# Kernel optimization log

Measured on AMD Instinct MI355X. Metric: run time of the kernel, lower is better.

Reference implementation:

```python
import jax, jax.numpy as jnp
import numpy as np

N = 50000       # node_num
E = 800000      # edges (no self loops; reference adds them)
IN_C = 128
OUT_C = 128
HEADS = 1
NEG_SLOPE = 0.2
BN_EPS = 1e-5


def setup_inputs() -> dict:
    key = jax.random.key(0)
    ks = jax.random.split(key, 12)
    x = jax.random.normal(ks[0], (N, IN_C), dtype=jnp.float32)
    # edge_index with no self-loops: dst = (src + off) % N, off in [1, N)
    src = jax.random.randint(ks[1], (E,), 0, N)
    off = jax.random.randint(ks[2], (E,), 1, N)
    dst = (src + off) % N
    edge_index = jnp.stack([src, dst]).astype(jnp.int64)
    embedding = jax.random.normal(ks[3], (N, OUT_C), dtype=jnp.float32)
    s = 1.0 / np.sqrt(IN_C)
    lin_w = jax.random.uniform(ks[4], (HEADS * OUT_C, IN_C), jnp.float32, -s, s)
    g = 0.1
    att_i = jax.random.normal(ks[5], (1, HEADS, OUT_C), jnp.float32) * g
    att_j = jax.random.normal(ks[6], (1, HEADS, OUT_C), jnp.float32) * g
    att_em_i = jax.random.normal(ks[7], (1, HEADS, OUT_C), jnp.float32) * g
    att_em_j = jax.random.normal(ks[8], (1, HEADS, OUT_C), jnp.float32) * g
    bias = jnp.zeros((OUT_C,), jnp.float32)
    gamma = jnp.ones((OUT_C,), jnp.float32)
    beta = jnp.zeros((OUT_C,), jnp.float32)
    return {"x": x, "edge_index": edge_index, "embedding": embedding,
            "lin_w": lin_w, "att_i": att_i, "att_j": att_j,
            "att_em_i": att_em_i, "att_em_j": att_em_j,
            "bias": bias, "gamma": gamma, "beta": beta}


def _gnn_forward(x, embedding, lin_w, att_i, att_j, att_em_i, att_em_j,
                 bias, gamma, beta, src, dst):
    n = x.shape[0]
    xl = (x @ lin_w.T).reshape(n, HEADS, OUT_C)          # [N,H,C]
    x_j = xl[src]                                         # [E',H,C] source
    x_i = xl[dst]                                         # [E',H,C] target
    emb_i = embedding[dst][:, None, :]                    # [E',1,C]
    emb_j = embedding[src][:, None, :]
    # alpha_e = <[x_i||emb_i], [att_i||att_em_i]> + <[x_j||emb_j], [att_j||att_em_j]>
    alpha = ((x_i * att_i).sum(-1) + (emb_i * att_em_i).sum(-1)
             + (x_j * att_j).sum(-1) + (emb_j * att_em_j).sum(-1))  # [E',H]
    alpha = jnp.where(alpha >= 0, alpha, NEG_SLOPE * alpha)         # leaky_relu
    # segment softmax over destination node (PyG softmax)
    amax = jax.ops.segment_max(alpha, dst, num_segments=n)
    ex = jnp.exp(alpha - amax[dst])
    denom = jax.ops.segment_sum(ex, dst, num_segments=n)
    alpha = ex / (denom[dst] + 1e-16)                               # [E',H]
    out = jax.ops.segment_sum(x_j * alpha[..., None], dst, num_segments=n)  # [N,H,C]
    out = out.mean(axis=1) + bias                                   # concat=False
    # BatchNorm1d, training mode (biased batch variance)
    mu = out.mean(axis=0)
    var = ((out - mu) ** 2).mean(axis=0)
    return (out - mu) * jax.lax.rsqrt(var + BN_EPS) * gamma + beta


def reference(x, edge_index, embedding, lin_w, att_i, att_j,
              att_em_i, att_em_j, bias, gamma, beta):
    n = x.shape[0]
    loops = jnp.arange(n, dtype=edge_index.dtype)
    src = jnp.concatenate([edge_index[0], loops])
    dst = jnp.concatenate([edge_index[1], loops])
    return _gnn_forward(x, embedding, lin_w, att_i, att_j, att_em_i,
                        att_em_j, bias, gamma, beta, src, dst)
```

## Files before the change

kernel.cpp:

```cpp
#include <hip/hip_runtime.h>

typedef short bf16x8 __attribute__((ext_vector_type(8)));
typedef float f32x4 __attribute__((ext_vector_type(4)));

__device__ __forceinline__ unsigned short f2bf(float f) {
  unsigned int u = __float_as_uint(f);
  u += 0x7fffu + ((u >> 16) & 1u);
  return (unsigned short)(u >> 16);
}
__device__ __forceinline__ float bf2f(unsigned short h) {
  return __uint_as_float(((unsigned int)h) << 16);
}
__device__ __forceinline__ float lrelu(float a) { return a >= 0.f ? a : 0.2f * a; }

#define BN_PS 1568

__global__ void zero_kernel(int* __restrict__ p, int n) {
  int i = blockIdx.x * blockDim.x + threadIdx.x;
  int stride = gridDim.x * blockDim.x;
  for (; i < n; i += stride) p[i] = 0;
}

__global__ __launch_bounds__(256) void gemm_kernel(
    const float* __restrict__ x, const float* __restrict__ w,
    const float* __restrict__ emb,
    const float* __restrict__ att_i, const float* __restrict__ att_j,
    const float* __restrict__ att_em_i, const float* __restrict__ att_em_j,
    unsigned short* __restrict__ xl, float* __restrict__ ai, float* __restrict__ aj,
    int n) {
  __shared__ __align__(16) unsigned short xs[64 * 128];
  __shared__ __align__(16) unsigned short wl[128 * 128];
  const int t = threadIdx.x;
  const int r0 = blockIdx.x * 64;
#pragma unroll
  for (int i = 0; i < 16; ++i) {
    int f4 = t + i * 256;
    int row = f4 >> 5;
    int kk = (f4 & 31) << 2;
    float4 v = *(const float4*)(w + row * 128 + kk);
    ushort4 b;
    b.x = f2bf(v.x); b.y = f2bf(v.y); b.z = f2bf(v.z); b.w = f2bf(v.w);
    int boff = (kk << 1) ^ ((row & 7) << 4);
    *(ushort4*)((char*)wl + row * 256 + boff) = b;
  }
#pragma unroll
  for (int i = 0; i < 8; ++i) {
    int f4 = t + i * 256;
    int row = f4 >> 5;
    int kk = (f4 & 31) << 2;
    int gr = r0 + row;
    float4 v;
    if (gr < n) v = *(const float4*)(x + gr * 128 + kk);
    else { v.x = 0.f; v.y = 0.f; v.z = 0.f; v.w = 0.f; }
    ushort4 b;
    b.x = f2bf(v.x); b.y = f2bf(v.y); b.z = f2bf(v.z); b.w = f2bf(v.w);
    int boff = (kk << 1) ^ ((row & 7) << 4);
    *(ushort4*)((char*)xs + row * 256 + boff) = b;
  }
  __syncthreads();
  const int wid = t >> 6, lane = t & 63;
  const int m16 = lane & 15, kg = lane >> 4;
  const int arow = wid * 16 + m16;
  const f32x4 vzero = {0.f, 0.f, 0.f, 0.f};
  f32x4 acc[8];
#pragma unroll
  for (int i = 0; i < 8; ++i) acc[i] = vzero;
#pragma unroll
  for (int s = 0; s < 4; ++s) {
    int kb = s * 64 + kg * 16;
    bf16x8 a = *(const bf16x8*)((const char*)xs + arow * 256 + (kb ^ ((arow & 7) << 4)));
#pragma unroll
    for (int cf = 0; cf < 8; ++cf) {
      int wrow = cf * 16 + m16;
      bf16x8 b = *(const bf16x8*)((const char*)wl + wrow * 256 + (kb ^ ((wrow & 7) << 4)));
      acc[cf] = __builtin_amdgcn_mfma_f32_16x16x32_bf16(a, b, acc[cf], 0, 0, 0);
    }
  }
  const int crow0 = wid * 16 + kg * 4;
#pragma unroll
  for (int q = 0; q < 4; ++q) {
    int gr = r0 + crow0 + q;
    if (gr < n) {
#pragma unroll
      for (int cf = 0; cf < 8; ++cf)
        xl[gr * 128 + cf * 16 + m16] = f2bf(acc[cf][q]);
    }
  }
  float ati[8], atj[8];
#pragma unroll
  for (int cf = 0; cf < 8; ++cf) {
    ati[cf] = att_i[cf * 16 + m16];
    atj[cf] = att_j[cf * 16 + m16];
  }
  float4 aemi0 = *(const float4*)(att_em_i + m16 * 8);
  float4 aemi1 = *(const float4*)(att_em_i + m16 * 8 + 4);
  float4 aemj0 = *(const float4*)(att_em_j + m16 * 8);
  float4 aemj1 = *(const float4*)(att_em_j + m16 * 8 + 4);
#pragma unroll
  for (int q = 0; q < 4; ++q) {
    int gr = r0 + crow0 + q;
    if (gr < n) {
      float si = 0.f, sj = 0.f;
#pragma unroll
      for (int cf = 0; cf < 8; ++cf) {
        si += acc[cf][q] * ati[cf];
        sj += acc[cf][q] * atj[cf];
      }
      const float* ep = emb + (size_t)gr * 128 + m16 * 8;
      float4 e0 = *(const float4*)(ep);
      float4 e1 = *(const float4*)(ep + 4);
      si += e0.x * aemi0.x + e0.y * aemi0.y + e0.z * aemi0.z + e0.w * aemi0.w
          + e1.x * aemi1.x + e1.y * aemi1.y + e1.z * aemi1.z + e1.w * aemi1.w;
      sj += e0.x * aemj0.x + e0.y * aemj0.y + e0.z * aemj0.z + e0.w * aemj0.w
          + e1.x * aemj1.x + e1.y * aemj1.y + e1.z * aemj1.z + e1.w * aemj1.w;
#pragma unroll
      for (int off = 1; off < 16; off <<= 1) {
        si += __shfl_xor(si, off);
        sj += __shfl_xor(sj, off);
      }
      if (m16 == 0) { ai[gr] = si; aj[gr] = sj; }
    }
  }
}

__global__ __launch_bounds__(256) void count_rank_kernel(
    const int* __restrict__ dst, int* __restrict__ cnt, int* __restrict__ pw, int E) {
  int e = (blockIdx.x * blockDim.x + threadIdx.x) * 4;
  if (e + 3 < E) {
    int4 d4 = *(const int4*)(dst + e);
    int4 p4;
    p4.x = atomicAdd(&cnt[d4.x], 1);
    p4.y = atomicAdd(&cnt[d4.y], 1);
    p4.z = atomicAdd(&cnt[d4.z], 1);
    p4.w = atomicAdd(&cnt[d4.w], 1);
    *(int4*)(pw + e) = p4;
  } else {
    for (; e < E; ++e) pw[e] = atomicAdd(&cnt[dst[e]], 1);
  }
}

__global__ __launch_bounds__(1024) void scan1_kernel(
    const int* __restrict__ cnt, int* __restrict__ rp, int* __restrict__ bsum, int n) {
  __shared__ int wsum[16];
  int t = threadIdx.x, lane = t & 63, wid = t >> 6;
  int i = blockIdx.x * 1024 + t;
  int v = (i < n) ? cnt[i] : 0;
  int incl = v;
#pragma unroll
  for (int off = 1; off < 64; off <<= 1) {
    int u = __shfl_up(incl, off);
    if (lane >= off) incl += u;
  }
  if (lane == 63) wsum[wid] = incl;
  __syncthreads();
  if (t < 16) {
    int wv = wsum[t];
    int winc = wv;
#pragma unroll
    for (int off = 1; off < 16; off <<= 1) {
      int u = __shfl_up(winc, off);
      if (t >= off) winc += u;
    }
    wsum[t] = winc - wv;
  }
  __syncthreads();
  int excl = wsum[wid] + incl - v;
  if (i < n) rp[i] = excl;
  if (t == 1023) bsum[blockIdx.x] = excl + v;
}

__global__ __launch_bounds__(64) void scan2_kernel(
    int* __restrict__ bsum, int* __restrict__ rp, int nb, int n) {
  int t = threadIdx.x;
  int carry = 0;
  for (int base = 0; base < nb; base += 64) {
    int idx = base + t;
    int v = (idx < nb) ? bsum[idx] : 0;
    int incl = v;
#pragma unroll
    for (int off = 1; off < 64; off <<= 1) {
      int u = __shfl_up(incl, off);
      if (t >= off) incl += u;
    }
    if (idx < nb) bsum[idx] = carry + incl - v;
    carry += __shfl(incl, 63);
  }
  if (t == 0) rp[n] = carry;
}

__global__ __launch_bounds__(256) void scan3_kernel(
    const int* __restrict__ bsum, int* __restrict__ rp, int n) {
  int i = blockIdx.x * blockDim.x + threadIdx.x;
  if (i < n) rp[i] += bsum[i >> 10];
}

__global__ __launch_bounds__(256) void scatter_kernel(
    const int* __restrict__ src, const int* __restrict__ dst,
    const int* __restrict__ rp, const int* __restrict__ pw,
    int* __restrict__ csr, int E) {
  int e = (blockIdx.x * blockDim.x + threadIdx.x) * 4;
  if (e + 3 < E) {
    int4 s4 = *(const int4*)(src + e);
    int4 d4 = *(const int4*)(dst + e);
    int4 p4 = *(const int4*)(pw + e);
    int r0 = rp[d4.x], r1 = rp[d4.y], r2 = rp[d4.z], r3 = rp[d4.w];
    csr[r0 + p4.x] = s4.x;
    csr[r1 + p4.y] = s4.y;
    csr[r2 + p4.z] = s4.z;
    csr[r3 + p4.w] = s4.w;
  } else {
    for (; e < E; ++e) csr[rp[dst[e]] + pw[e]] = src[e];
  }
}

__global__ __launch_bounds__(256) void agg_kernel(
    const float* __restrict__ ai, const float* __restrict__ aj,
    const unsigned short* __restrict__ xl,
    const int* __restrict__ row_ptr, const int* __restrict__ csr_src,
    const float* __restrict__ bias, float* __restrict__ out, int n) {
  int wid = threadIdx.x >> 6, lane = threadIdx.x & 63;
  int node = blockIdx.x * 4 + wid;
  if (node >= n) return;
  int beg = row_ptr[node], end = row_ptr[node + 1];
  float ain = ai[node];
  float w_self = __expf(lrelu(ain + aj[node]));
  float dl = 0.f;
  float acc0 = 0.f, acc1 = 0.f;
  const int c0 = lane * 2;
  for (int cs = beg; cs < end; cs += 64) {
    int ce = min(64, end - cs);
    int s = 0;
    float we = 0.f;
    if (lane < ce) {
      s = csr_src[cs + lane];
      we = __expf(lrelu(ain + aj[s]));
    }
    dl += we;
    int j = 0;
    for (; j + 8 <= ce; j += 8) {
      float w0 = __shfl(we, j),     w1 = __shfl(we, j + 1);
      float w2 = __shfl(we, j + 2), w3 = __shfl(we, j + 3);
      float w4 = __shfl(we, j + 4), w5 = __shfl(we, j + 5);
      float w6 = __shfl(we, j + 6), w7 = __shfl(we, j + 7);
      int i0 = __shfl(s, j),     i1 = __shfl(s, j + 1);
      int i2 = __shfl(s, j + 2), i3 = __shfl(s, j + 3);
      int i4 = __shfl(s, j + 4), i5 = __shfl(s, j + 5);
      int i6 = __shfl(s, j + 6), i7 = __shfl(s, j + 7);
      ushort2 v0 = *(const ushort2*)(xl + (size_t)i0 * 128 + c0);
      ushort2 v1 = *(const ushort2*)(xl + (size_t)i1 * 128 + c0);
      ushort2 v2 = *(const ushort2*)(xl + (size_t)i2 * 128 + c0);
      ushort2 v3 = *(const ushort2*)(xl + (size_t)i3 * 128 + c0);
      ushort2 v4 = *(const ushort2*)(xl + (size_t)i4 * 128 + c0);
      ushort2 v5 = *(const ushort2*)(xl + (size_t)i5 * 128 + c0);
      ushort2 v6 = *(const ushort2*)(xl + (size_t)i6 * 128 + c0);
      ushort2 v7 = *(const ushort2*)(xl + (size_t)i7 * 128 + c0);
      acc0 += w0 * bf2f(v0.x); acc1 += w0 * bf2f(v0.y);
      acc0 += w1 * bf2f(v1.x); acc1 += w1 * bf2f(v1.y);
      acc0 += w2 * bf2f(v2.x); acc1 += w2 * bf2f(v2.y);
      acc0 += w3 * bf2f(v3.x); acc1 += w3 * bf2f(v3.y);
      acc0 += w4 * bf2f(v4.x); acc1 += w4 * bf2f(v4.y);
      acc0 += w5 * bf2f(v5.x); acc1 += w5 * bf2f(v5.y);
      acc0 += w6 * bf2f(v6.x); acc1 += w6 * bf2f(v6.y);
      acc0 += w7 * bf2f(v7.x); acc1 += w7 * bf2f(v7.y);
    }
    for (; j < ce; ++j) {
      float wj = __shfl(we, j);
      int ij = __shfl(s, j);
      ushort2 v = *(const ushort2*)(xl + (size_t)ij * 128 + c0);
      acc0 += wj * bf2f(v.x); acc1 += wj * bf2f(v.y);
    }
  }
#pragma unroll
  for (int off = 32; off > 0; off >>= 1) dl += __shfl_xor(dl, off);
  float inv = 1.f / (dl + w_self + 1e-16f);
  ushort2 u = *(const ushort2*)(xl + (size_t)node * 128 + c0);
  float2 o;
  o.x = (acc0 + w_self * bf2f(u.x)) * inv + bias[c0];
  o.y = (acc1 + w_self * bf2f(u.y)) * inv + bias[c0 + 1];
  *(float2*)(out + (size_t)node * 128 + c0) = o;
}

__global__ __launch_bounds__(256) void bnstat_a_kernel(
    const float* __restrict__ out, float* __restrict__ pS, float* __restrict__ pQ,
    int n) {
  __shared__ float4 red_s[8][32];
  __shared__ float4 red_q[8][32];
  int q = threadIdx.x & 31;
  int rs = threadIdx.x >> 5;
  int rbase = blockIdx.x * 32;
  float4 s = {0.f, 0.f, 0.f, 0.f}, ss = {0.f, 0.f, 0.f, 0.f};
#pragma unroll
  for (int k = 0; k < 4; ++k) {
    int r = rbase + rs + k * 8;
    if (r < n) {
      float4 v = *(const float4*)(out + (size_t)r * 128 + q * 4);
      s.x += v.x; s.y += v.y; s.z += v.z; s.w += v.w;
      ss.x += v.x * v.x; ss.y += v.y * v.y; ss.z += v.z * v.z; ss.w += v.w * v.w;
    }
  }
  red_s[rs][q] = s;
  red_q[rs][q] = ss;
  __syncthreads();
  if (threadIdx.x < 32) {
    float4 ts = red_s[0][threadIdx.x], tq = red_q[0][threadIdx.x];
#pragma unroll
    for (int k = 1; k < 8; ++k) {
      float4 a = red_s[k][threadIdx.x], b = red_q[k][threadIdx.x];
      ts.x += a.x; ts.y += a.y; ts.z += a.z; ts.w += a.w;
      tq.x += b.x; tq.y += b.y; tq.z += b.z; tq.w += b.w;
    }
    int c = threadIdx.x * 4;
    int b = blockIdx.x;
    pS[(c + 0) * BN_PS + b] = ts.x; pS[(c + 1) * BN_PS + b] = ts.y;
    pS[(c + 2) * BN_PS + b] = ts.z; pS[(c + 3) * BN_PS + b] = ts.w;
    pQ[(c + 0) * BN_PS + b] = tq.x; pQ[(c + 1) * BN_PS + b] = tq.y;
    pQ[(c + 2) * BN_PS + b] = tq.z; pQ[(c + 3) * BN_PS + b] = tq.w;
  }
}

__global__ __launch_bounds__(256) void bnstat_b_kernel(
    const float* __restrict__ pS, const float* __restrict__ pQ,
    float* __restrict__ sums, float* __restrict__ sumsq, int nb) {
  __shared__ float ws_s[4], ws_q[4];
  int c = blockIdx.x;
  int t = threadIdx.x, lane = t & 63, wid = t >> 6;
  const float* rowS = pS + (size_t)c * BN_PS;
  const float* rowQ = pQ + (size_t)c * BN_PS;
  float s = 0.f, qv = 0.f;
  for (int i = t; i < nb; i += 256) {
    s += rowS[i];
    qv += rowQ[i];
  }
#pragma unroll
  for (int off = 32; off > 0; off >>= 1) {
    s += __shfl_xor(s, off);
    qv += __shfl_xor(qv, off);
  }
  if (lane == 0) { ws_s[wid] = s; ws_q[wid] = qv; }
  __syncthreads();
  if (t == 0) {
    sums[c] = ws_s[0] + ws_s[1] + ws_s[2] + ws_s[3];
    sumsq[c] = ws_q[0] + ws_q[1] + ws_q[2] + ws_q[3];
  }
}

__global__ __launch_bounds__(256) void bnapply_kernel(
    float* __restrict__ out, const float* __restrict__ sums,
    const float* __restrict__ sumsq, const float* __restrict__ gamma,
    const float* __restrict__ beta, int n, float invN) {
  int q = threadIdx.x & 31;
  int rs = threadIdx.x >> 5;
  int c = q * 4;
  float4 mu, var, sc, sh;
  mu.x = sums[c + 0] * invN; mu.y = sums[c + 1] * invN;
  mu.z = sums[c + 2] * invN; mu.w = sums[c + 3] * invN;
  var.x = sumsq[c + 0] * invN - mu.x * mu.x;
  var.y = sumsq[c + 1] * invN - mu.y * mu.y;
  var.z = sumsq[c + 2] * invN - mu.z * mu.z;
  var.w = sumsq[c + 3] * invN - mu.w * mu.w;
  sc.x = rsqrtf(var.x + 1e-5f) * gamma[c + 0];
  sc.y = rsqrtf(var.y + 1e-5f) * gamma[c + 1];
  sc.z = rsqrtf(var.z + 1e-5f) * gamma[c + 2];
  sc.w = rsqrtf(var.w + 1e-5f) * gamma[c + 3];
  sh.x = beta[c + 0] - mu.x * sc.x;
  sh.y = beta[c + 1] - mu.y * sc.y;
  sh.z = beta[c + 2] - mu.z * sc.z;
  sh.w = beta[c + 3] - mu.w * sc.w;
  for (int r = blockIdx.x * 8 + rs; r < n; r += gridDim.x * 8) {
    float4 v = *(const float4*)(out + (size_t)r * 128 + c);
    v.x = v.x * sc.x + sh.x;
    v.y = v.y * sc.y + sh.y;
    v.z = v.z * sc.z + sh.z;
    v.w = v.w * sc.w + sh.w;
    *(float4*)(out + (size_t)r * 128 + c) = v;
  }
}

extern "C" void kernel_launch(void* const* d_in, const int* in_sizes, int n_in,
                              void* d_out, int out_size, void* d_ws, size_t ws_size,
                              hipStream_t stream) {
  (void)n_in; (void)out_size; (void)ws_size;
  const float* x = (const float*)d_in[0];
  const int* ei = (const int*)d_in[1];
  const float* emb = (const float*)d_in[2];
  const float* lin_w = (const float*)d_in[3];
  const float* att_i = (const float*)d_in[4];
  const float* att_j = (const float*)d_in[5];
  const float* att_em_i = (const float*)d_in[6];
  const float* att_em_j = (const float*)d_in[7];
  const float* bias = (const float*)d_in[8];
  const float* gamma = (const float*)d_in[9];
  const float* beta = (const float*)d_in[10];
  float* out = (float*)d_out;
  const int N = in_sizes[0] / 128;
  const int E = in_sizes[1] / 2;
  const int* src = ei;
  const int* dst = ei + E;
  const int NB = (N + 1023) / 1024;
  const int NBA = (N + 31) / 32;

  auto align_up = [](size_t v) { return (v + 255) & ~(size_t)255; };
  size_t off = 0;
  size_t xl_off = off;    off = align_up(off + (size_t)N * 128 * 2);
  size_t ai_off = off;    off = align_up(off + (size_t)N * 4);
  size_t aj_off = off;    off = align_up(off + (size_t)N * 4);
  size_t rp_off = off;    off = align_up(off + (size_t)(N + 1) * 4);
  size_t csr_off = off;   off = align_up(off + (size_t)E * 4);
  size_t pw_off = off;    off = align_up(off + (size_t)E * 4);
  size_t bsum_off = off;  off = align_up(off + (size_t)(NB + 1) * 4);
  size_t pS_off = off;    off = align_up(off + (size_t)128 * BN_PS * 4);
  size_t pQ_off = off;    off = align_up(off + (size_t)128 * BN_PS * 4);
  size_t sums_off = off;  off = align_up(off + 512);
  size_t sumsq_off = off; off = align_up(off + 512);
  size_t cnt_off = off;   off = align_up(off + (size_t)N * 4);

  char* ws = (char*)d_ws;
  unsigned short* xl = (unsigned short*)(ws + xl_off);
  float* ai = (float*)(ws + ai_off);
  float* aj = (float*)(ws + aj_off);
  int* rp = (int*)(ws + rp_off);
  int* csr = (int*)(ws + csr_off);
  int* pw = (int*)(ws + pw_off);
  int* bsum = (int*)(ws + bsum_off);
  float* pS = (float*)(ws + pS_off);
  float* pQ = (float*)(ws + pQ_off);
  float* sums = (float*)(ws + sums_off);
  float* sumsq = (float*)(ws + sumsq_off);
  int* cnt = (int*)(ws + cnt_off);

  hipLaunchKernelGGL(zero_kernel, dim3((N + 255) / 256), dim3(256), 0, stream,
                     cnt, N);
  hipLaunchKernelGGL(gemm_kernel, dim3((N + 63) / 64), dim3(256), 0, stream,
                     x, lin_w, emb, att_i, att_j, att_em_i, att_em_j,
                     xl, ai, aj, N);
  hipLaunchKernelGGL(count_rank_kernel, dim3((E / 4 + 255) / 256), dim3(256), 0, stream,
                     dst, cnt, pw, E);
  hipLaunchKernelGGL(scan1_kernel, dim3(NB), dim3(1024), 0, stream, cnt, rp, bsum, N);
  hipLaunchKernelGGL(scan2_kernel, dim3(1), dim3(64), 0, stream, bsum, rp, NB, N);
  hipLaunchKernelGGL(scan3_kernel, dim3((N + 255) / 256), dim3(256), 0, stream,
                     bsum, rp, N);
  hipLaunchKernelGGL(scatter_kernel, dim3((E / 4 + 255) / 256), dim3(256), 0, stream,
                     src, dst, rp, pw, csr, E);
  hipLaunchKernelGGL(agg_kernel, dim3((N + 3) / 4), dim3(256), 0, stream,
                     ai, aj, xl, rp, csr, bias, out, N);
  hipLaunchKernelGGL(bnstat_a_kernel, dim3(NBA), dim3(256), 0, stream,
                     out, pS, pQ, N);
  hipLaunchKernelGGL(bnstat_b_kernel, dim3(128), dim3(256), 0, stream,
                     pS, pQ, sums, sumsq, NBA);
  hipLaunchKernelGGL(bnapply_kernel, dim3(2048), dim3(256), 0, stream,
                     out, sums, sumsq, gamma, beta, N, 1.0f / (float)N);
}
```

Before: 240.2 us.

## Fuse edge counting into GEMM launch, merge scans, fold BN stats into aggregation

Edge-count atomics now run as extra blocks of the GEMM kernel, so both overlap in one launch. The two-stage block-prefix scan is merged into a single kernel where each block recomputes its prefix with wave reductions. BatchNorm partial sums are computed inside the aggregation kernel, which removes a full reread of the output. It also prefetches the next CSR chunk and widens scatter to 8 edges per thread. The cost is redundant per-block prefix work and a larger partial-sum buffer (one entry per 4 nodes) for bnstat_b to reduce.

```diff
diff --git a/kernel.cpp b/kernel.cpp
--- a/kernel.cpp
+++ b/kernel.cpp
@@ -13,23 +13,44 @@
 }
 __device__ __forceinline__ float lrelu(float a) { return a >= 0.f ? a : 0.2f * a; }
 
-#define BN_PS 1568
-
 __global__ void zero_kernel(int* __restrict__ p, int n) {
   int i = blockIdx.x * blockDim.x + threadIdx.x;
   int stride = gridDim.x * blockDim.x;
   for (; i < n; i += stride) p[i] = 0;
 }
 
-__global__ __launch_bounds__(256) void gemm_kernel(
+__global__ __launch_bounds__(256) void gemm_cnt_kernel(
     const float* __restrict__ x, const float* __restrict__ w,
     const float* __restrict__ emb,
     const float* __restrict__ att_i, const float* __restrict__ att_j,
     const float* __restrict__ att_em_i, const float* __restrict__ att_em_j,
     unsigned short* __restrict__ xl, float* __restrict__ ai, float* __restrict__ aj,
-    int n) {
+    int n,
+    const int* __restrict__ dst, int* __restrict__ cnt, int* __restrict__ pw, int E,
+    int NBG) {
   __shared__ __align__(16) unsigned short xs[64 * 128];
   __shared__ __align__(16) unsigned short wl[128 * 128];
+  if (blockIdx.x >= NBG) {
+    int e = ((blockIdx.x - NBG) * blockDim.x + threadIdx.x) * 8;
+    if (e + 8 <= E) {
+      int4 d0 = *(const int4*)(dst + e);
+      int4 d1 = *(const int4*)(dst + e + 4);
+      int4 p0, p1;
+      p0.x = atomicAdd(&cnt[d0.x], 1);
+      p0.y = atomicAdd(&cnt[d0.y], 1);
+      p0.z = atomicAdd(&cnt[d0.z], 1);
+      p0.w = atomicAdd(&cnt[d0.w], 1);
+      p1.x = atomicAdd(&cnt[d1.x], 1);
+      p1.y = atomicAdd(&cnt[d1.y], 1);
+      p1.z = atomicAdd(&cnt[d1.z], 1);
+      p1.w = atomicAdd(&cnt[d1.w], 1);
+      *(int4*)(pw + e) = p0;
+      *(int4*)(pw + e + 4) = p1;
+    } else {
+      for (; e < E; ++e) pw[e] = atomicAdd(&cnt[dst[e]], 1);
+    }
+    return;
+  }
   const int t = threadIdx.x;
   const int r0 = blockIdx.x * 64;
 #pragma unroll
@@ -123,22 +144,6 @@
   }
 }
 
-__global__ __launch_bounds__(256) void count_rank_kernel(
-    const int* __restrict__ dst, int* __restrict__ cnt, int* __restrict__ pw, int E) {
-  int e = (blockIdx.x * blockDim.x + threadIdx.x) * 4;
-  if (e + 3 < E) {
-    int4 d4 = *(const int4*)(dst + e);
-    int4 p4;
-    p4.x = atomicAdd(&cnt[d4.x], 1);
-    p4.y = atomicAdd(&cnt[d4.y], 1);
-    p4.z = atomicAdd(&cnt[d4.z], 1);
-    p4.w = atomicAdd(&cnt[d4.w], 1);
-    *(int4*)(pw + e) = p4;
-  } else {
-    for (; e < E; ++e) pw[e] = atomicAdd(&cnt[dst[e]], 1);
-  }
-}
-
 __global__ __launch_bounds__(1024) void scan1_kernel(
     const int* __restrict__ cnt, int* __restrict__ rp, int* __restrict__ bsum, int n) {
   __shared__ int wsum[16];
@@ -169,45 +174,50 @@
   if (t == 1023) bsum[blockIdx.x] = excl + v;
 }
 
-__global__ __launch_bounds__(64) void scan2_kernel(
-    int* __restrict__ bsum, int* __restrict__ rp, int nb, int n) {
-  int t = threadIdx.x;
-  int carry = 0;
+__global__ __launch_bounds__(256) void scan3_kernel(
+    const int* __restrict__ bsum, int* __restrict__ rp, int n, int nb) {
+  int lane = threadIdx.x & 63;
+  int bb = blockIdx.x >> 2;
+  int pref = 0, tot = 0;
   for (int base = 0; base < nb; base += 64) {
-    int idx = base + t;
+    int idx = base + lane;
     int v = (idx < nb) ? bsum[idx] : 0;
-    int incl = v;
-#pragma unroll
-    for (int off = 1; off < 64; off <<= 1) {
-      int u = __shfl_up(incl, off);
-      if (t >= off) incl += u;
-    }
-    if (idx < nb) bsum[idx] = carry + incl - v;
-    carry += __shfl(incl, 63);
-  }
-  if (t == 0) rp[n] = carry;
-}
-
-__global__ __launch_bounds__(256) void scan3_kernel(
-    const int* __restrict__ bsum, int* __restrict__ rp, int n) {
-  int i = blockIdx.x * blockDim.x + threadIdx.x;
-  if (i < n) rp[i] += bsum[i >> 10];
+    int p = (idx < bb) ? v : 0;
+#pragma unroll
+    for (int off = 32; off > 0; off >>= 1) {
+      p += __shfl_xor(p, off);
+      v += __shfl_xor(v, off);
+    }
+    pref += p;
+    tot += v;
+  }
+  int i = blockIdx.x * 256 + threadIdx.x;
+  if (i < n) rp[i] += pref;
+  if (blockIdx.x == gridDim.x - 1 && threadIdx.x == 0) rp[n] = tot;
 }
 
 __global__ __launch_bounds__(256) void scatter_kernel(
     const int* __restrict__ src, const int* __restrict__ dst,
     const int* __restrict__ rp, const int* __restrict__ pw,
     int* __restrict__ csr, int E) {
-  int e = (blockIdx.x * blockDim.x + threadIdx.x) * 4;
-  if (e + 3 < E) {
-    int4 s4 = *(const int4*)(src + e);
-    int4 d4 = *(const int4*)(dst + e);
-    int4 p4 = *(const int4*)(pw + e);
-    int r0 = rp[d4.x], r1 = rp[d4.y], r2 = rp[d4.z], r3 = rp[d4.w];
-    csr[r0 + p4.x] = s4.x;
-    csr[r1 + p4.y] = s4.y;
-    csr[r2 + p4.z] = s4.z;
-    csr[r3 + p4.w] = s4.w;
+  int e = (blockIdx.x * blockDim.x + threadIdx.x) * 8;
+  if (e + 8 <= E) {
+    int4 s0 = *(const int4*)(src + e);
+    int4 s1 = *(const int4*)(src + e + 4);
+    int4 d0 = *(const int4*)(dst + e);
+    int4 d1 = *(const int4*)(dst + e + 4);
+    int4 p0 = *(const int4*)(pw + e);
+    int4 p1 = *(const int4*)(pw + e + 4);
+    int r0 = rp[d0.x], r1 = rp[d0.y], r2 = rp[d0.z], r3 = rp[d0.w];
+    int r4 = rp[d1.x], r5 = rp[d1.y], r6 = rp[d1.z], r7 = rp[d1.w];
+    csr[r0 + p0.x] = s0.x;
+    csr[r1 + p0.y] = s0.y;
+    csr[r2 + p0.z] = s0.z;
+    csr[r3 + p0.w] = s0.w;
+    csr[r4 + p1.x] = s1.x;
+    csr[r5 + p1.y] = s1.y;
+    csr[r6 + p1.z] = s1.z;
+    csr[r7 + p1.w] = s1.w;
   } else {
     for (; e < E; ++e) csr[rp[dst[e]] + pw[e]] = src[e];
   }
@@ -217,25 +227,32 @@
     const float* __restrict__ ai, const float* __restrict__ aj,
     const unsigned short* __restrict__ xl,
     const int* __restrict__ row_ptr, const int* __restrict__ csr_src,
-    const float* __restrict__ bias, float* __restrict__ out, int n) {
+    const float* __restrict__ bias, float* __restrict__ out,
+    float* __restrict__ pS, float* __restrict__ pQ, int n, int ps2) {
+  __shared__ float2 red_s[4][64];
+  __shared__ float2 red_q[4][64];
   int wid = threadIdx.x >> 6, lane = threadIdx.x & 63;
   int node = blockIdx.x * 4 + wid;
-  if (node >= n) return;
-  int beg = row_ptr[node], end = row_ptr[node + 1];
-  float ain = ai[node];
-  float w_self = __expf(lrelu(ain + aj[node]));
-  float dl = 0.f;
-  float acc0 = 0.f, acc1 = 0.f;
+  bool active = node < n;
+  int beg = 0, end = 0;
+  float ain = 0.f, w_self = 0.f;
+  if (active) {
+    beg = row_ptr[node];
+    end = row_ptr[node + 1];
+    ain = ai[node];
+    w_self = __expf(lrelu(ain + aj[node]));
+  }
+  float dl = 0.f, acc0 = 0.f, acc1 = 0.f;
   const int c0 = lane * 2;
+  int s = 0;
+  if (beg + lane < end) s = csr_src[beg + lane];
   for (int cs = beg; cs < end; cs += 64) {
     int ce = min(64, end - cs);
-    int s = 0;
     float we = 0.f;
-    if (lane < ce) {
-      s = csr_src[cs + lane];
-      we = __expf(lrelu(ain + aj[s]));
-    }
+    if (lane < ce) we = __expf(lrelu(ain + aj[s]));
     dl += we;
+    int s_nxt = 0;
+    if (cs + 64 + lane < end) s_nxt = csr_src[cs + 64 + lane];
     int j = 0;
     for (; j + 8 <= ce; j += 8) {
       float w0 = __shfl(we, j),     w1 = __shfl(we, j + 1);
@@ -269,63 +286,47 @@
       ushort2 v = *(const ushort2*)(xl + (size_t)ij * 128 + c0);
       acc0 += wj * bf2f(v.x); acc1 += wj * bf2f(v.y);
     }
+    s = s_nxt;
   }
 #pragma unroll
   for (int off = 32; off > 0; off >>= 1) dl += __shfl_xor(dl, off);
   float inv = 1.f / (dl + w_self + 1e-16f);
-  ushort2 u = *(const ushort2*)(xl + (size_t)node * 128 + c0);
-  float2 o;
-  o.x = (acc0 + w_self * bf2f(u.x)) * inv + bias[c0];
-  o.y = (acc1 + w_self * bf2f(u.y)) * inv + bias[c0 + 1];
-  *(float2*)(out + (size_t)node * 128 + c0) = o;
-}
-
-__global__ __launch_bounds__(256) void bnstat_a_kernel(
-    const float* __restrict__ out, float* __restrict__ pS, float* __restrict__ pQ,
-    int n) {
-  __shared__ float4 red_s[8][32];
-  __shared__ float4 red_q[8][32];
-  int q = threadIdx.x & 31;
-  int rs = threadIdx.x >> 5;
-  int rbase = blockIdx.x * 32;
-  float4 s = {0.f, 0.f, 0.f, 0.f}, ss = {0.f, 0.f, 0.f, 0.f};
-#pragma unroll
-  for (int k = 0; k < 4; ++k) {
-    int r = rbase + rs + k * 8;
-    if (r < n) {
-      float4 v = *(const float4*)(out + (size_t)r * 128 + q * 4);
-      s.x += v.x; s.y += v.y; s.z += v.z; s.w += v.w;
-      ss.x += v.x * v.x; ss.y += v.y * v.y; ss.z += v.z * v.z; ss.w += v.w * v.w;
-    }
-  }
-  red_s[rs][q] = s;
-  red_q[rs][q] = ss;
+  float2 o; o.x = 0.f; o.y = 0.f;
+  if (active) {
+    ushort2 u = *(const ushort2*)(xl + (size_t)node * 128 + c0);
+    o.x = (acc0 + w_self * bf2f(u.x)) * inv + bias[c0];
+    o.y = (acc1 + w_self * bf2f(u.y)) * inv + bias[c0 + 1];
+    *(float2*)(out + (size_t)node * 128 + c0) = o;
+  }
+  red_s[wid][lane] = o;
+  float2 oq; oq.x = o.x * o.x; oq.y = o.y * o.y;
+  red_q[wid][lane] = oq;
   __syncthreads();
-  if (threadIdx.x < 32) {
-    float4 ts = red_s[0][threadIdx.x], tq = red_q[0][threadIdx.x];
-#pragma unroll
-    for (int k = 1; k < 8; ++k) {
-      float4 a = red_s[k][threadIdx.x], b = red_q[k][threadIdx.x];
-      ts.x += a.x; ts.y += a.y; ts.z += a.z; ts.w += a.w;
-      tq.x += b.x; tq.y += b.y; tq.z += b.z; tq.w += b.w;
-    }
-    int c = threadIdx.x * 4;
-    int b = blockIdx.x;
-    pS[(c + 0) * BN_PS + b] = ts.x; pS[(c + 1) * BN_PS + b] = ts.y;
-    pS[(c + 2) * BN_PS + b] = ts.z; pS[(c + 3) * BN_PS + b] = ts.w;
-    pQ[(c + 0) * BN_PS + b] = tq.x; pQ[(c + 1) * BN_PS + b] = tq.y;
-    pQ[(c + 2) * BN_PS + b] = tq.z; pQ[(c + 3) * BN_PS + b] = tq.w;
+  int t = threadIdx.x;
+  if (t < 128) {
+    int l = t >> 1, cm = t & 1;
+    float ssum = 0.f;
+#pragma unroll
+    for (int w = 0; w < 4; ++w) ssum += cm ? red_s[w][l].y : red_s[w][l].x;
+    pS[(size_t)t * ps2 + blockIdx.x] = ssum;
+  } else {
+    int tt = t - 128;
+    int l = tt >> 1, cm = tt & 1;
+    float qsum = 0.f;
+#pragma unroll
+    for (int w = 0; w < 4; ++w) qsum += cm ? red_q[w][l].y : red_q[w][l].x;
+    pQ[(size_t)tt * ps2 + blockIdx.x] = qsum;
   }
 }
 
 __global__ __launch_bounds__(256) void bnstat_b_kernel(
     const float* __restrict__ pS, const float* __restrict__ pQ,
-    float* __restrict__ sums, float* __restrict__ sumsq, int nb) {
+    float* __restrict__ sums, float* __restrict__ sumsq, int nb, int ps2) {
   __shared__ float ws_s[4], ws_q[4];
   int c = blockIdx.x;
   int t = threadIdx.x, lane = t & 63, wid = t >> 6;
-  const float* rowS = pS + (size_t)c * BN_PS;
-  const float* rowQ = pQ + (size_t)c * BN_PS;
+  const float* rowS = pS + (size_t)c * ps2;
+  const float* rowQ = pQ + (size_t)c * ps2;
   float s = 0.f, qv = 0.f;
   for (int i = t; i < nb; i += 256) {
     s += rowS[i];
@@ -397,7 +398,10 @@
   const int* src = ei;
   const int* dst = ei + E;
   const int NB = (N + 1023) / 1024;
-  const int NBA = (N + 31) / 32;
+  const int NBG = (N + 63) / 64;
+  const int NBC = (E / 8 + 255) / 256 + 1;
+  const int NBAG = (N + 3) / 4;
+  const int PS2 = ((NBAG + 63) / 64) * 64;
 
   auto align_up = [](size_t v) { return (v + 255) & ~(size_t)255; };
   size_t off = 0;
@@ -408,8 +412,8 @@
   size_t csr_off = off;   off = align_up(off + (size_t)E * 4);
   size_t pw_off = off;    off = align_up(off + (size_t)E * 4);
   size_t bsum_off = off;  off = align_up(off + (size_t)(NB + 1) * 4);
-  size_t pS_off = off;    off = align_up(off + (size_t)128 * BN_PS * 4);
-  size_t pQ_off = off;    off = align_up(off + (size_t)128 * BN_PS * 4);
+  size_t pS_off = off;    off = align_up(off + (size_t)128 * PS2 * 4);
+  size_t pQ_off = off;    off = align_up(off + (size_t)128 * PS2 * 4);
   size_t sums_off = off;  off = align_up(off + 512);
   size_t sumsq_off = off; off = align_up(off + 512);
   size_t cnt_off = off;   off = align_up(off + (size_t)N * 4);
@@ -430,23 +434,18 @@
 
   hipLaunchKernelGGL(zero_kernel, dim3((N + 255) / 256), dim3(256), 0, stream,
                      cnt, N);
-  hipLaunchKernelGGL(gemm_kernel, dim3((N + 63) / 64), dim3(256), 0, stream,
+  hipLaunchKernelGGL(gemm_cnt_kernel, dim3(NBG + NBC), dim3(256), 0, stream,
                      x, lin_w, emb, att_i, att_j, att_em_i, att_em_j,
-                     xl, ai, aj, N);
-  hipLaunchKernelGGL(count_rank_kernel, dim3((E / 4 + 255) / 256), dim3(256), 0, stream,
-                     dst, cnt, pw, E);
+                     xl, ai, aj, N, dst, cnt, pw, E, NBG);
   hipLaunchKernelGGL(scan1_kernel, dim3(NB), dim3(1024), 0, stream, cnt, rp, bsum, N);
-  hipLaunchKernelGGL(scan2_kernel, dim3(1), dim3(64), 0, stream, bsum, rp, NB, N);
   hipLaunchKernelGGL(scan3_kernel, dim3((N + 255) / 256), dim3(256), 0, stream,
-                     bsum, rp, N);
-  hipLaunchKernelGGL(scatter_kernel, dim3((E / 4 + 255) / 256), dim3(256), 0, stream,
-                     src, dst, rp, pw, csr, E);
-  hipLaunchKernelGGL(agg_kernel, dim3((N + 3) / 4), dim3(256), 0, stream,
-                     ai, aj, xl, rp, csr, bias, out, N);
-  hipLaunchKernelGGL(bnstat_a_kernel, dim3(NBA), dim3(256), 0, stream,
-                     out, pS, pQ, N);
+                     bsum, rp, N, NB);
+  hipLaunchKernelGGL(scatter_kernel, dim3((E / 8 + 255) / 256 + 1), dim3(256), 0,
+                     stream, src, dst, rp, pw, csr, E);
+  hipLaunchKernelGGL(agg_kernel, dim3(NBAG), dim3(256), 0, stream,
+                     ai, aj, xl, rp, csr, bias, out, pS, pQ, N, PS2);
   hipLaunchKernelGGL(bnstat_b_kernel, dim3(128), dim3(256), 0, stream,
-                     pS, pQ, sums, sumsq, NBA);
+                     pS, pQ, sums, sumsq, NBAG, PS2);
   hipLaunchKernelGGL(bnapply_kernel, dim3(2048), dim3(256), 0, stream,
                      out, sums, sumsq, gamma, beta, N, 1.0f / (float)N);
 }
```

New measurement: 265.1 us. 10.4% more time.
